# Kernel optimization log

Hardware: AMD Instinct MI355X
Metric: run time of the kernel (lower is better)

The kernel has to match this reference:

```python
import jax, jax.numpy as jnp
import numpy as np

B, S, H = 1, 2048, 2048
NH, NKV, HD = 32, 8, 64
RBS, ICS, RBN = 64, 64, 16          # retrieval_block_size, input_chunk_size, retrieval_block_num
RLEN = RBS * RBN                     # 1024 retrieval tokens
KV = RLEN + S                        # 3072 total kv length
START = RLEN                         # INPUT_START_IDX
SCALE = HD ** -0.5
NEG = -1e9


def _document_ids():
    # mirrors get_document_ids
    ids = np.full(KV, -1, np.int32)
    ids[:START] = np.arange(START) // RBS + 1            # retrieval blocks -> 1..RBN
    chunk = np.arange(S) // ICS
    ids[START:] = np.where(chunk == 0, -1, np.minimum(chunk, RBN))
    return ids


def _block_mask():
    # mirrors causal_retrieval_mask_mod, precomputed dense [S, KV]
    ids = _document_ids()
    qpos = np.arange(S) + START
    kv = np.arange(KV)
    causal = (qpos[:, None] >= kv[None, :]) & (kv[None, :] > START)
    doc = (ids[qpos][:, None] == ids[None, :]) & (kv[None, :] < START)
    return jnp.asarray(causal | doc)


_MASK = _block_mask()


def _rotate_half(x):
    h = x.shape[-1] // 2
    return jnp.concatenate([-x[..., h:], x[..., :h]], axis=-1)


def setup_inputs() -> dict:
    key = jax.random.key(0)
    ks = jax.random.split(key, 6)
    inv_freq = 1.0 / (10000.0 ** (np.arange(0, HD, 2, dtype=np.float32) / HD))
    ang = np.arange(S, dtype=np.float32)[:, None] * inv_freq[None, :]   # [S, HD/2]
    emb = np.concatenate([ang, ang], axis=-1)                            # [S, HD]
    cos = jnp.asarray(np.cos(emb))[None].astype(jnp.float32)            # [1, S, HD]
    sin = jnp.asarray(np.sin(emb))[None].astype(jnp.float32)
    return {
        "hidden_states": jax.random.normal(ks[0], (B, S, H), jnp.float32),
        "cos": cos,
        "sin": sin,
        "retrieval_key": jax.random.normal(ks[1], (B, NKV, RLEN, HD), jnp.float32),
        "retrieval_value": jax.random.normal(ks[2], (B, NKV, RLEN, HD), jnp.float32),
        "Wq": jax.random.normal(ks[3], (H, NH * HD), jnp.float32) * 0.02,
        "Wk": jax.random.normal(ks[4], (H, NKV * HD), jnp.float32) * 0.02,
        "Wv": jax.random.normal(ks[5], (H, NKV * HD), jnp.float32) * 0.02,
        "Wo": jax.random.normal(jax.random.fold_in(key, 7), (NH * HD, H), jnp.float32) * 0.02,
    }


def reference(hidden_states, cos, sin, retrieval_key, retrieval_value, Wq, Wk, Wv, Wo):
    # QKV projections -> [B, nheads, S, HD]
    q = (hidden_states @ Wq).reshape(B, S, NH, HD).transpose(0, 2, 1, 3)
    k = (hidden_states @ Wk).reshape(B, S, NKV, HD).transpose(0, 2, 1, 3)
    v = (hidden_states @ Wv).reshape(B, S, NKV, HD).transpose(0, 2, 1, 3)
    # RoPE (retrieval kv is pre-encoded; rope only on current tokens)
    c, s = cos[:, None, :, :], sin[:, None, :, :]
    q = q * c + _rotate_half(q) * s
    k = k * c + _rotate_half(k) * s
    # prepend retrieval kv
    k = jnp.concatenate([retrieval_key, k], axis=2)    # [B, NKV, KV, HD]
    v = jnp.concatenate([retrieval_value, v], axis=2)
    # GQA: expand kv heads
    g = NH // NKV
    k = jnp.repeat(k, g, axis=1)                        # [B, NH, KV, HD]
    v = jnp.repeat(v, g, axis=1)
    scores = jnp.einsum("bhqd,bhkd->bhqk", q, k) * SCALE
    scores = jnp.where(_MASK[None, None], scores, NEG)
    probs = jax.nn.softmax(scores, axis=-1)
    # fully-masked rows (q_idx 0) -> zero output, matching flex_attention
    row_valid = _MASK.any(axis=-1)[None, None, :, None]
    probs = jnp.where(row_valid, probs, 0.0)
    out = jnp.einsum("bhqk,bhkd->bhqd", probs, v)
    out = out.transpose(0, 2, 1, 3).reshape(B, S, NH * HD)
    return out @ Wo
```

## Files before the change

kernel.cpp:

```cpp
#include <hip/hip_runtime.h>

#define S_LEN 2048
#define H_DIM 2048
#define NH 32
#define NKV 8
#define HD 64
#define RLEN 1024
#define KVTOT 3072
#define SCALE 0.125f
#define QS 0.18033688011112042f
#define FIX8 11.541560327111707f

typedef unsigned short ushort_t;
using short8 = __attribute__((ext_vector_type(8))) short;
using f32x4 = __attribute__((ext_vector_type(4))) float;

__device__ __forceinline__ float b2f(unsigned short u) {
    union { unsigned int i; float f; } v;
    v.i = ((unsigned int)u) << 16;
    return v.f;
}
__device__ __forceinline__ unsigned short f2b(float f) {
    union { float f; unsigned int i; } v;
    v.f = f;
    unsigned int x = v.i;
    return (unsigned short)((x + 0x7fffu + ((x >> 16) & 1u)) >> 16);
}

__device__ __forceinline__ uint4 ld8(const void* A, size_t idx, int F) {
    if (F) {
        const float* p = (const float*)A + idx;
        float4 f0 = ((const float4*)p)[0], f1 = ((const float4*)p)[1];
        ushort_t o[8];
        o[0] = f2b(f0.x); o[1] = f2b(f0.y); o[2] = f2b(f0.z); o[3] = f2b(f0.w);
        o[4] = f2b(f1.x); o[5] = f2b(f1.y); o[6] = f2b(f1.z); o[7] = f2b(f1.w);
        return *(uint4*)o;
    }
    return *(const uint4*)((const ushort_t*)A + idx);
}

__global__ void detect9(const void* p0, const void* p1, const void* p2,
                        const void* p3, const void* p4, const void* p5,
                        const void* p6, const void* p7, const void* p8,
                        int* flags)
{
    __shared__ int bad;
    if (threadIdx.x == 0) bad = 0;
    __syncthreads();
    const void* ps[9] = {p0, p1, p2, p3, p4, p5, p6, p7, p8};
    const unsigned int* w = (const unsigned int*)ps[blockIdx.x];
    int cnt = 0;
    for (int i = threadIdx.x; i < 4096; i += blockDim.x) {
        unsigned int lo = w[i] & 0xFFFFu;
        unsigned int e = (lo >> 7) & 0xFFu;
        if (lo != 0u && (e < 90u || e > 140u)) ++cnt;
    }
    atomicAdd(&bad, cnt);
    __syncthreads();
    if (threadIdx.x == 0) flags[blockIdx.x] = (bad > 16) ? 1 : 0;
}

__global__ __launch_bounds__(256) void cvtW(
    const void* __restrict__ Wq, const void* __restrict__ Wk,
    const void* __restrict__ Wv, const void* __restrict__ Wo,
    ushort_t* __restrict__ WqkvT, ushort_t* __restrict__ WoT,
    const int* __restrict__ flags)
{
    const int z = blockIdx.z;
    if ((z == 1 || z == 2) && blockIdx.x >= 8) return;
    const void* src = (z == 0) ? Wq : (z == 1) ? Wk : (z == 2) ? Wv : Wo;
    const int F = flags[5 + z];
    const int C = (z == 1 || z == 2) ? 512 : 2048;
    ushort_t* dst = (z == 3) ? WoT : WqkvT;
    const int rofs = (z == 1) ? 2048 : (z == 2) ? 2560 : 0;

    __shared__ ushort_t S[64 * 72];
    const int r0 = blockIdx.y * 64, c0 = blockIdx.x * 64;
    const int lr = threadIdx.x >> 2, lc = (threadIdx.x & 3) * 16;
    size_t base = (size_t)(r0 + lr) * C + c0 + lc;
    *(uint4*)&S[lr * 72 + lc] = ld8(src, base, F);
    *(uint4*)&S[lr * 72 + lc + 8] = ld8(src, base + 8, F);
    __syncthreads();
    const int wc = threadIdx.x >> 2, wr = (threadIdx.x & 3) * 16;
    ushort_t o[16];
#pragma unroll
    for (int j = 0; j < 16; ++j) o[j] = S[(wr + j) * 72 + wc];
    ushort_t* q = dst + (size_t)(rofs + c0 + wc) * 2048 + r0 + wr;
    *(uint4*)q = *(const uint4*)o;
    *(uint4*)(q + 8) = *(const uint4*)(o + 8);
}

__global__ __launch_bounds__(256) void gemm_qkv(
    const void* __restrict__ A, const ushort_t* __restrict__ Bt,
    ushort_t* __restrict__ C, int N, int K, const int* __restrict__ aF_)
{
    const int aF = *aF_;
    __shared__ __align__(16) ushort_t As[2][64 * 40];
    __shared__ __align__(16) ushort_t Bs[2][128 * 40];
    const int tid = threadIdx.x;
    const int wave = tid >> 6, lane = tid & 63;
    const int lq = lane & 15, quad = lane >> 4;
    const int m0 = blockIdx.y * 64, n0 = blockIdx.x * 128;
    const int wm = (wave & 1) * 32, wn = (wave >> 1) * 64;
    const int ar = tid >> 2, ak = (tid & 3) * 8;
    const int br = tid >> 1, bk = (tid & 1) * 16;
    const int nk = K >> 5;

    f32x4 acc[2][4];
#pragma unroll
    for (int i = 0; i < 2; ++i)
#pragma unroll
        for (int j = 0; j < 4; ++j) acc[i][j] = (f32x4){0.f, 0.f, 0.f, 0.f};

    const size_t aidx = (size_t)(m0 + ar) * K + ak;
    const ushort_t* bp = Bt + (size_t)(n0 + br) * K + bk;
    {
        uint4 a0 = ld8(A, aidx, aF);
        uint4 b0 = ((const uint4*)bp)[0], b1 = ((const uint4*)bp)[1];
        *(uint4*)&As[0][ar * 40 + ak] = a0;
        *(uint4*)&Bs[0][br * 40 + bk] = b0; *(uint4*)&Bs[0][br * 40 + bk + 8] = b1;
    }

    for (int kt = 0; kt < nk; ++kt) {
        const int cur = kt & 1;
        uint4 na0, nb0, nb1;
        const bool more = (kt + 1 < nk);
        if (more) {
            na0 = ld8(A, aidx + (kt + 1) * 32, aF);
            const ushort_t* bp2 = bp + (kt + 1) * 32;
            nb0 = ((const uint4*)bp2)[0]; nb1 = ((const uint4*)bp2)[1];
        }
        __syncthreads();
        short8 afr[2], bfr[4];
#pragma unroll
        for (int i = 0; i < 2; ++i)
            afr[i] = *(const short8*)&As[cur][(wm + i * 16 + lq) * 40 + quad * 8];
#pragma unroll
        for (int j = 0; j < 4; ++j)
            bfr[j] = *(const short8*)&Bs[cur][(wn + j * 16 + lq) * 40 + quad * 8];
#pragma unroll
        for (int i = 0; i < 2; ++i)
#pragma unroll
            for (int j = 0; j < 4; ++j)
                acc[i][j] = __builtin_amdgcn_mfma_f32_16x16x32_bf16(afr[i], bfr[j], acc[i][j], 0, 0, 0);
        __syncthreads();
        if (more) {
            const int nxt = cur ^ 1;
            *(uint4*)&As[nxt][ar * 40 + ak] = na0;
            *(uint4*)&Bs[nxt][br * 40 + bk] = nb0; *(uint4*)&Bs[nxt][br * 40 + bk + 8] = nb1;
        }
    }

#pragma unroll
    for (int i = 0; i < 2; ++i)
#pragma unroll
        for (int r = 0; r < 4; ++r) {
            ushort_t* cp = C + (size_t)(m0 + wm + i * 16 + quad * 4 + r) * N + n0 + wn + lq;
#pragma unroll
            for (int j = 0; j < 4; ++j) cp[j * 16] = f2b(acc[i][j][r]);
        }
}

__global__ __launch_bounds__(256) void gemm_fin(
    const ushort_t* __restrict__ A, const ushort_t* __restrict__ Bt,
    void* __restrict__ Cv, int N, int K, const int* __restrict__ oF_)
{
    const int oF = *oF_;
    __shared__ __align__(16) ushort_t As[2][64 * 40];
    __shared__ __align__(16) ushort_t Bs[2][128 * 40];
    const int tid = threadIdx.x;
    const int wave = tid >> 6, lane = tid & 63;
    const int lq = lane & 15, quad = lane >> 4;
    const int m0 = blockIdx.y * 64, n0 = blockIdx.x * 128;
    const int wm = (wave & 1) * 32, wn = (wave >> 1) * 64;
    const int ar = tid >> 2, ak = (tid & 3) * 8;
    const int br = tid >> 1, bk = (tid & 1) * 16;
    const int nk = K >> 5;

    f32x4 acc[2][4];
#pragma unroll
    for (int i = 0; i < 2; ++i)
#pragma unroll
        for (int j = 0; j < 4; ++j) acc[i][j] = (f32x4){0.f, 0.f, 0.f, 0.f};

    const ushort_t* ap = A + (size_t)(m0 + ar) * K + ak;
    const ushort_t* bp = Bt + (size_t)(n0 + br) * K + bk;
    {
        uint4 a0 = ((const uint4*)ap)[0];
        uint4 b0 = ((const uint4*)bp)[0], b1 = ((const uint4*)bp)[1];
        *(uint4*)&As[0][ar * 40 + ak] = a0;
        *(uint4*)&Bs[0][br * 40 + bk] = b0; *(uint4*)&Bs[0][br * 40 + bk + 8] = b1;
    }

    for (int kt = 0; kt < nk; ++kt) {
        const int cur = kt & 1;
        uint4 na0, nb0, nb1;
        const bool more = (kt + 1 < nk);
        if (more) {
            na0 = *(const uint4*)(ap + (kt + 1) * 32);
            const ushort_t* bp2 = bp + (kt + 1) * 32;
            nb0 = ((const uint4*)bp2)[0]; nb1 = ((const uint4*)bp2)[1];
        }
        __syncthreads();
        short8 afr[2], bfr[4];
#pragma unroll
        for (int i = 0; i < 2; ++i)
            afr[i] = *(const short8*)&As[cur][(wm + i * 16 + lq) * 40 + quad * 8];
#pragma unroll
        for (int j = 0; j < 4; ++j)
            bfr[j] = *(const short8*)&Bs[cur][(wn + j * 16 + lq) * 40 + quad * 8];
#pragma unroll
        for (int i = 0; i < 2; ++i)
#pragma unroll
            for (int j = 0; j < 4; ++j)
                acc[i][j] = __builtin_amdgcn_mfma_f32_16x16x32_bf16(afr[i], bfr[j], acc[i][j], 0, 0, 0);
        __syncthreads();
        if (more) {
            const int nxt = cur ^ 1;
            *(uint4*)&As[nxt][ar * 40 + ak] = na0;
            *(uint4*)&Bs[nxt][br * 40 + bk] = nb0; *(uint4*)&Bs[nxt][br * 40 + bk + 8] = nb1;
        }
    }

#pragma unroll
    for (int i = 0; i < 2; ++i)
#pragma unroll
        for (int r = 0; r < 4; ++r) {
            size_t off = (size_t)(m0 + wm + i * 16 + quad * 4 + r) * N + n0 + wn + lq;
            if (oF) {
                float* cp = (float*)Cv + off;
#pragma unroll
                for (int j = 0; j < 4; ++j) cp[j * 16] = acc[i][j][r];
            } else {
                ushort_t* cp = (ushort_t*)Cv + off;
#pragma unroll
                for (int j = 0; j < 4; ++j) cp[j * 16] = f2b(acc[i][j][r]);
            }
        }
}

__global__ __launch_bounds__(256) void prepKV(
    const void* __restrict__ rk, const void* __restrict__ rv,
    const ushort_t* __restrict__ qkvp,
    const void* __restrict__ cosv, const void* __restrict__ sinv,
    ushort_t* __restrict__ ktall, ushort_t* __restrict__ vtall,
    const int* __restrict__ flags)
{
    if (blockIdx.z == 0) {
        const int vF = flags[4];
        const int t = blockIdx.x;
        const int kvh = blockIdx.y;
        __shared__ ushort_t S[64 * 72];
        const int lr = threadIdx.x >> 2, lc = (threadIdx.x & 3) * 16;
        if (t < 16) {
            size_t base = ((size_t)kvh * RLEN + t * 64 + lr) * HD + lc;
            *(uint4*)&S[lr * 72 + lc] = ld8(rv, base, vF);
            *(uint4*)&S[lr * 72 + lc + 8] = ld8(rv, base + 8, vF);
        } else {
            const ushort_t* p = qkvp + (size_t)((t - 16) * 64 + lr) * 3072 + 2560 + kvh * HD + lc;
            *(uint4*)&S[lr * 72 + lc] = ((const uint4*)p)[0];
            *(uint4*)&S[lr * 72 + lc + 8] = ((const uint4*)p)[1];
        }
        __syncthreads();
        const int wc = threadIdx.x >> 2, wr = (threadIdx.x & 3) * 16;
        ushort_t o[16];
#pragma unroll
        for (int j = 0; j < 16; ++j) o[j] = S[(wr + j) * 72 + wc];
        const int blk = t * 2 + (wr >> 5);
        ushort_t* q = vtall + (((size_t)(kvh * 96 + blk) * 64 + wc) * 32) + (wr & 31);
        *(uint4*)q = *(const uint4*)o;
        *(uint4*)(q + 8) = *(const uint4*)(o + 8);
    } else {
        const int kF = flags[3], cF = flags[1], sF = flags[2];
        int flat = (blockIdx.y * 48 + blockIdx.x) * 256 + threadIdx.x;
        const int d0 = (flat & 3) * 8;
        const int p = (flat >> 2) % KVTOT;
        const int kvh = (flat >> 2) / KVTOT;
        ushort_t o0[8], o1[8];
        if (p < RLEN) {
            size_t base = ((size_t)kvh * RLEN + p) * HD;
            *(uint4*)o0 = ld8(rk, base + d0, kF);
            *(uint4*)o1 = ld8(rk, base + d0 + 32, kF);
        } else {
            const int si = p - RLEN;
            const ushort_t* s = qkvp + (size_t)si * 3072 + 2048 + kvh * HD;
            uint4 u0 = *(const uint4*)(s + d0);
            uint4 u1 = *(const uint4*)(s + d0 + 32);
            const ushort_t* a16 = (const ushort_t*)&u0;
            const ushort_t* b16 = (const ushort_t*)&u1;
            int ci = si * HD + d0;
            float c0[8], c1[8], s0[8], s1[8];
            if (cF) {
                const float* cp = (const float*)cosv + ci;
#pragma unroll
                for (int j = 0; j < 8; ++j) { c0[j] = cp[j]; c1[j] = cp[j + 32]; }
            } else {
                const ushort_t* cp = (const ushort_t*)cosv + ci;
#pragma unroll
                for (int j = 0; j < 8; ++j) { c0[j] = b2f(cp[j]); c1[j] = b2f(cp[j + 32]); }
            }
            if (sF) {
                const float* sp = (const float*)sinv + ci;
#pragma unroll
                for (int j = 0; j < 8; ++j) { s0[j] = sp[j]; s1[j] = sp[j + 32]; }
            } else {
                const ushort_t* sp = (const ushort_t*)sinv + ci;
#pragma unroll
                for (int j = 0; j < 8; ++j) { s0[j] = b2f(sp[j]); s1[j] = b2f(sp[j + 32]); }
            }
#pragma unroll
            for (int j = 0; j < 8; ++j) {
                float a = b2f(a16[j]), b = b2f(b16[j]);
                o0[j] = f2b(a * c0[j] - b * s0[j]);
                o1[j] = f2b(b * c1[j] + a * s1[j]);
            }
        }
        ushort_t* q = ktall + ((size_t)kvh * KVTOT + p) * HD;
        *(uint4*)(q + d0) = *(const uint4*)o0;
        *(uint4*)(q + d0 + 32) = *(const uint4*)o1;
    }
}

__global__ __launch_bounds__(256) void fattn(
    const ushort_t* __restrict__ qkvp, const ushort_t* __restrict__ ktall,
    const ushort_t* __restrict__ vtall, ushort_t* __restrict__ attno,
    const void* __restrict__ cosv, const void* __restrict__ sinv,
    const int* __restrict__ flags)
{
    const int cF = flags[1], sF = flags[2];
    const int h = blockIdx.x;
    const int qb = 31 - blockIdx.y;
    const int kvh = h >> 2;
    const int tid = threadIdx.x;
    const int wave = tid >> 6;
    const int lane = tid & 63;
    const int lq = lane & 15;
    const int quad = lane >> 4;
    const int rb64 = ((qb < 17 ? qb : 16) - 1) * 64;

    __shared__ __align__(16) ushort_t Ks[128 * 72];
    __shared__ __align__(16) ushort_t Ps[4 * 16 * 136];
    ushort_t* pw = &Ps[wave * 16 * 136];

    short8 qfrag[2];
    {
        const int row_g = qb * 64 + wave * 16 + lq;
        const ushort_t* qrow = qkvp + (size_t)row_g * 3072 + h * HD;
        short8 t0 = *(const short8*)(qrow + quad * 8);
        short8 t1 = *(const short8*)(qrow + 32 + quad * 8);
        const int ci = row_g * HD + quad * 8;
        float c0[8], c1[8], s0[8], s1[8];
        if (cF) {
            const float* cp = (const float*)cosv + ci;
#pragma unroll
            for (int j = 0; j < 8; ++j) { c0[j] = cp[j]; c1[j] = cp[j + 32]; }
        } else {
            const ushort_t* cp = (const ushort_t*)cosv + ci;
#pragma unroll
            for (int j = 0; j < 8; ++j) { c0[j] = b2f(cp[j]); c1[j] = b2f(cp[j + 32]); }
        }
        if (sF) {
            const float* sp = (const float*)sinv + ci;
#pragma unroll
            for (int j = 0; j < 8; ++j) { s0[j] = sp[j]; s1[j] = sp[j + 32]; }
        } else {
            const ushort_t* sp = (const ushort_t*)sinv + ci;
#pragma unroll
            for (int j = 0; j < 8; ++j) { s0[j] = b2f(sp[j]); s1[j] = b2f(sp[j + 32]); }
        }
#pragma unroll
        for (int j = 0; j < 8; ++j) {
            float a = b2f((unsigned short)t0[j]), b = b2f((unsigned short)t1[j]);
            qfrag[0][j] = (short)f2b((a * c0[j] - b * s0[j]) * QS);
            qfrag[1][j] = (short)f2b((b * c1[j] + a * s1[j]) * QS);
        }
    }

    f32x4 oacc[4];
#pragma unroll
    for (int nt = 0; nt < 4; ++nt) oacc[nt] = (f32x4){0.f, 0.f, 0.f, 0.f};
    float lsum[4] = {0.f, 0.f, 0.f, 0.f};

    const int Lq = (qb > 0) ? qb * 64 + 128 : 64;
    const int nch = (Lq + 127) >> 7;
    const ushort_t* kbase = ktall + (size_t)kvh * KVTOT * HD;
    const ushort_t* vbase = vtall + (size_t)kvh * 96 * 2048;

    const int krow = tid >> 1;
    const int kd0 = (tid & 1) * 32;

    uint4 kreg0, kreg1, kreg2, kreg3;
    {
        uint4 z = {0, 0, 0, 0};
        kreg0 = z; kreg1 = z; kreg2 = z; kreg3 = z;
        int p = krow;
        if (p < Lq) {
            int pk = (qb > 0) ? ((p < 64) ? rb64 + p : 960 + p) : RLEN + p;
            const uint4* s = (const uint4*)(kbase + (size_t)pk * HD + kd0);
            kreg0 = s[0]; kreg1 = s[1]; kreg2 = s[2]; kreg3 = s[3];
        }
    }

    for (int c = 0; c < nch; ++c) {
        {
            uint4* dk = (uint4*)&Ks[krow * 72 + kd0];
            dk[0] = kreg0; dk[1] = kreg1; dk[2] = kreg2; dk[3] = kreg3;
        }
        __syncthreads();

        if (c + 1 < nch) {
            uint4 z = {0, 0, 0, 0};
            kreg0 = z; kreg1 = z; kreg2 = z; kreg3 = z;
            int p = (c + 1) * 128 + krow;
            if (p < Lq) {
                int pk = (qb > 0) ? ((p < 64) ? rb64 + p : 960 + p) : RLEN + p;
                const uint4* s = (const uint4*)(kbase + (size_t)pk * HD + kd0);
                kreg0 = s[0]; kreg1 = s[1]; kreg2 = s[2]; kreg3 = s[3];
            }
        }

        int vblk[4];
#pragma unroll
        for (int kc = 0; kc < 4; ++kc) {
            int p = c * 128 + kc * 32;
            int pk = (qb > 0) ? ((p < 64) ? rb64 + p : 960 + p) : RLEN + p;
            if (pk > KVTOT - 1) pk = KVTOT - 1;
            vblk[kc] = pk >> 5;
        }
        short8 vfA[4], vfB[4];
#pragma unroll
        for (int ntd = 0; ntd < 4; ++ntd)
            vfA[ntd] = *(const short8*)(vbase + ((size_t)vblk[0] * 64 + ntd * 16 + lq) * 32 + quad * 8);
#pragma unroll
        for (int ntd = 0; ntd < 4; ++ntd)
            vfB[ntd] = *(const short8*)(vbase + ((size_t)vblk[1] * 64 + ntd * 16 + lq) * 32 + quad * 8);

        const bool lastc = (c == nch - 1) || (qb == 0);
#pragma unroll
        for (int nt = 0; nt < 8; ++nt) {
            f32x4 a = (f32x4){0.f, 0.f, 0.f, 0.f};
            a = __builtin_amdgcn_mfma_f32_16x16x32_bf16(qfrag[0],
                *(const short8*)&Ks[(nt * 16 + lq) * 72 + quad * 8], a, 0, 0, 0);
            a = __builtin_amdgcn_mfma_f32_16x16x32_bf16(qfrag[1],
                *(const short8*)&Ks[(nt * 16 + lq) * 72 + 32 + quad * 8], a, 0, 0, 0);
            const int p = c * 128 + nt * 16 + lq;
#pragma unroll
            for (int r = 0; r < 4; ++r) {
                float pexp = exp2f(a[r] - FIX8);
                if (lastc) {
                    const int qg = qb * 64 + wave * 16 + quad * 4 + r;
                    bool valid;
                    if (qb > 0) valid = (p < 64) || ((p - 64) >= 1 && (p - 64) <= qg);
                    else        valid = (p >= 1 && p <= qg);
                    if (!valid) pexp = 0.f;
                } else if (c == 0) {
                    if (p == 64) pexp = 0.f;
                }
                lsum[r] += pexp;
                pw[(quad * 4 + r) * 136 + nt * 16 + lq] = f2b(pexp);
            }
        }

#pragma unroll
        for (int kc = 0; kc < 4; ++kc) {
            short8 pa = *(const short8*)&pw[lq * 136 + kc * 32 + quad * 8];
            short8 vf0, vf1, vf2, vf3;
            if (kc == 0)      { vf0 = vfA[0]; vf1 = vfA[1]; vf2 = vfA[2]; vf3 = vfA[3]; }
            else if (kc == 1) { vf0 = vfB[0]; vf1 = vfB[1]; vf2 = vfB[2]; vf3 = vfB[3]; }
            else {
                const int b = vblk[kc];
                vf0 = *(const short8*)(vbase + ((size_t)b * 64 + 0 * 16 + lq) * 32 + quad * 8);
                vf1 = *(const short8*)(vbase + ((size_t)b * 64 + 1 * 16 + lq) * 32 + quad * 8);
                vf2 = *(const short8*)(vbase + ((size_t)b * 64 + 2 * 16 + lq) * 32 + quad * 8);
                vf3 = *(const short8*)(vbase + ((size_t)b * 64 + 3 * 16 + lq) * 32 + quad * 8);
            }
            oacc[0] = __builtin_amdgcn_mfma_f32_16x16x32_bf16(pa, vf0, oacc[0], 0, 0, 0);
            oacc[1] = __builtin_amdgcn_mfma_f32_16x16x32_bf16(pa, vf1, oacc[1], 0, 0, 0);
            oacc[2] = __builtin_amdgcn_mfma_f32_16x16x32_bf16(pa, vf2, oacc[2], 0, 0, 0);
            oacc[3] = __builtin_amdgcn_mfma_f32_16x16x32_bf16(pa, vf3, oacc[3], 0, 0, 0);
        }
        __syncthreads();
    }

#pragma unroll
    for (int r = 0; r < 4; ++r) {
        float v = lsum[r];
        v += __shfl_xor(v, 1, 64); v += __shfl_xor(v, 2, 64);
        v += __shfl_xor(v, 4, 64); v += __shfl_xor(v, 8, 64);
        lsum[r] = v;
    }
#pragma unroll
    for (int r = 0; r < 4; ++r) {
        const int qg = qb * 64 + wave * 16 + quad * 4 + r;
        const float inv = (qg == 0) ? 0.f : 1.f / lsum[r];
        ushort_t* orow = attno + (size_t)qg * 2048 + h * HD;
#pragma unroll
        for (int nt = 0; nt < 4; ++nt)
            orow[nt * 16 + lq] = f2b(oacc[nt][r] * inv);
    }
}

extern "C" void kernel_launch(void* const* d_in, const int* in_sizes, int n_in,
                              void* d_out, int out_size, void* d_ws, size_t ws_size,
                              hipStream_t stream) {
    const void* hs   = d_in[0];
    const void* cosv = d_in[1];
    const void* sinv = d_in[2];
    const void* rk   = d_in[3];
    const void* rv   = d_in[4];
    const void* Wq   = d_in[5];
    const void* Wk   = d_in[6];
    const void* Wv   = d_in[7];
    const void* Wo   = d_in[8];

    char* ws = (char*)d_ws;
    int*      flags  = (int*)ws;
    ushort_t* ktall  = (ushort_t*)(ws + (1u  << 20));
    ushort_t* vtall  = (ushort_t*)(ws + (1u << 20) + (13u << 18));
    ushort_t* WqkvT  = (ushort_t*)(ws + (9u  << 20));
    ushort_t* attno  = WqkvT;
    ushort_t* WoT    = (ushort_t*)(ws + (21u << 20));
    ushort_t* qkvp   = (ushort_t*)(ws + (29u << 20));

    detect9<<<9, 256, 0, stream>>>(hs, cosv, sinv, rk, rv, Wq, Wk, Wv, Wo, flags);

    cvtW<<<dim3(32, 32, 4), 256, 0, stream>>>(Wq, Wk, Wv, Wo, WqkvT, WoT, flags);

    gemm_qkv<<<dim3(3072 / 128, 2048 / 64), 256, 0, stream>>>(hs, WqkvT, qkvp, 3072, 2048, flags + 0);

    prepKV<<<dim3(48, 8, 2), 256, 0, stream>>>(rk, rv, qkvp, cosv, sinv, ktall, vtall, flags);

    fattn<<<dim3(NH, 32), 256, 0, stream>>>(qkvp, ktall, vtall, attno, cosv, sinv, flags);

    gemm_fin<<<dim3(2048 / 128, 2048 / 64), 256, 0, stream>>>(attno, WoT, d_out, 2048, 2048, flags + 0);
}
```

Before: 288.6 us.

## Split long query blocks' KV range across two workgroups with a reduce kernel

Query blocks 16..31, which have the longest KV ranges, are each split into two workgroups that process halves of the KV chunks. One half writes unnormalized partial outputs into attno and the other into a scratch buffer, and both write their row sums to Lbuf. A new freduce kernel then adds the partials and normalizes them. This balances per-workgroup work and raises the workgroup count, at the cost of an extra launch, partial outputs rounded to bf16, and the loss of the register prefetch of the next K chunk, which is now loaded synchronously each iteration. The fixed exponent offset in place of a running max makes combining the partials by simple addition valid.

```diff
diff --git a/kernel.cpp b/kernel.cpp
--- a/kernel.cpp
+++ b/kernel.cpp
@@ -324,12 +324,31 @@
 __global__ __launch_bounds__(256) void fattn(
     const ushort_t* __restrict__ qkvp, const ushort_t* __restrict__ ktall,
     const ushort_t* __restrict__ vtall, ushort_t* __restrict__ attno,
+    ushort_t* __restrict__ part, float* __restrict__ Lbuf,
     const void* __restrict__ cosv, const void* __restrict__ sinv,
     const int* __restrict__ flags)
 {
     const int cF = flags[1], sF = flags[2];
     const int h = blockIdx.x;
-    const int qb = 31 - blockIdx.y;
+    const int y = blockIdx.y;
+    int qb, cBeg, cEnd, split, slice;
+    {
+        if (y < 32) {
+            qb = 31 - (y >> 1);
+            slice = y & 1;
+            split = 1;
+            const int nch = ((qb * 64 + 128) + 127) >> 7;
+            const int half = nch >> 1;
+            cBeg = slice ? half : 0;
+            cEnd = slice ? nch : half;
+        } else {
+            qb = 47 - y;
+            slice = 0; split = 0;
+            cBeg = 0;
+            cEnd = (qb > 0) ? (((qb * 64 + 128) + 127) >> 7) : 1;
+        }
+    }
+    const int nchTot = (qb > 0) ? (((qb * 64 + 128) + 127) >> 7) : 1;
     const int kvh = h >> 2;
     const int tid = threadIdx.x;
     const int wave = tid >> 6;
@@ -382,43 +401,23 @@
     float lsum[4] = {0.f, 0.f, 0.f, 0.f};
 
     const int Lq = (qb > 0) ? qb * 64 + 128 : 64;
-    const int nch = (Lq + 127) >> 7;
     const ushort_t* kbase = ktall + (size_t)kvh * KVTOT * HD;
     const ushort_t* vbase = vtall + (size_t)kvh * 96 * 2048;
 
-    const int krow = tid >> 1;
-    const int kd0 = (tid & 1) * 32;
-
-    uint4 kreg0, kreg1, kreg2, kreg3;
-    {
-        uint4 z = {0, 0, 0, 0};
-        kreg0 = z; kreg1 = z; kreg2 = z; kreg3 = z;
-        int p = krow;
-        if (p < Lq) {
-            int pk = (qb > 0) ? ((p < 64) ? rb64 + p : 960 + p) : RLEN + p;
-            const uint4* s = (const uint4*)(kbase + (size_t)pk * HD + kd0);
-            kreg0 = s[0]; kreg1 = s[1]; kreg2 = s[2]; kreg3 = s[3];
-        }
-    }
-
-    for (int c = 0; c < nch; ++c) {
+    for (int c = cBeg; c < cEnd; ++c) {
+        uint4 kreg0, kreg1, kreg2, kreg3;
+        const int krow = tid >> 1;
+        const int kd0 = (tid & 1) * 32;
         {
-            uint4* dk = (uint4*)&Ks[krow * 72 + kd0];
-            dk[0] = kreg0; dk[1] = kreg1; dk[2] = kreg2; dk[3] = kreg3;
-        }
-        __syncthreads();
-
-        if (c + 1 < nch) {
+            int p = c * 128 + krow;
             uint4 z = {0, 0, 0, 0};
             kreg0 = z; kreg1 = z; kreg2 = z; kreg3 = z;
-            int p = (c + 1) * 128 + krow;
             if (p < Lq) {
                 int pk = (qb > 0) ? ((p < 64) ? rb64 + p : 960 + p) : RLEN + p;
                 const uint4* s = (const uint4*)(kbase + (size_t)pk * HD + kd0);
                 kreg0 = s[0]; kreg1 = s[1]; kreg2 = s[2]; kreg3 = s[3];
             }
         }
-
         int vblk[4];
 #pragma unroll
         for (int kc = 0; kc < 4; ++kc) {
@@ -435,7 +434,13 @@
         for (int ntd = 0; ntd < 4; ++ntd)
             vfB[ntd] = *(const short8*)(vbase + ((size_t)vblk[1] * 64 + ntd * 16 + lq) * 32 + quad * 8);
 
-        const bool lastc = (c == nch - 1) || (qb == 0);
+        {
+            uint4* dk = (uint4*)&Ks[krow * 72 + kd0];
+            dk[0] = kreg0; dk[1] = kreg1; dk[2] = kreg2; dk[3] = kreg3;
+        }
+        __syncthreads();
+
+        const bool lastc = (c == nchTot - 1) || (qb == 0);
 #pragma unroll
         for (int nt = 0; nt < 8; ++nt) {
             f32x4 a = (f32x4){0.f, 0.f, 0.f, 0.f};
@@ -489,15 +494,58 @@
         v += __shfl_xor(v, 4, 64); v += __shfl_xor(v, 8, 64);
         lsum[r] = v;
     }
-#pragma unroll
-    for (int r = 0; r < 4; ++r) {
-        const int qg = qb * 64 + wave * 16 + quad * 4 + r;
-        const float inv = (qg == 0) ? 0.f : 1.f / lsum[r];
-        ushort_t* orow = attno + (size_t)qg * 2048 + h * HD;
-#pragma unroll
-        for (int nt = 0; nt < 4; ++nt)
-            orow[nt * 16 + lq] = f2b(oacc[nt][r] * inv);
-    }
+    if (!split) {
+#pragma unroll
+        for (int r = 0; r < 4; ++r) {
+            const int qg = qb * 64 + wave * 16 + quad * 4 + r;
+            const float inv = (qg == 0) ? 0.f : 1.f / lsum[r];
+            ushort_t* orow = attno + (size_t)qg * 2048 + h * HD;
+#pragma unroll
+            for (int nt = 0; nt < 4; ++nt)
+                orow[nt * 16 + lq] = f2b(oacc[nt][r] * inv);
+        }
+    } else {
+        const int pidx = h * 16 + (qb - 16);
+#pragma unroll
+        for (int r = 0; r < 4; ++r) {
+            const int row = wave * 16 + quad * 4 + r;
+            ushort_t* orow = slice ? (part + (size_t)pidx * 4096 + row * 64)
+                                   : (attno + (size_t)(qb * 64 + row) * 2048 + h * HD);
+#pragma unroll
+            for (int nt = 0; nt < 4; ++nt)
+                orow[nt * 16 + lq] = f2b(oacc[nt][r]);
+            if (lq == 0)
+                Lbuf[(pidx * 2 + slice) * 64 + row] = lsum[r];
+        }
+    }
+}
+
+__global__ __launch_bounds__(256) void freduce(
+    ushort_t* __restrict__ attno, const ushort_t* __restrict__ part,
+    const float* __restrict__ Lbuf)
+{
+    const int idx = blockIdx.x;
+    const int h = idx >> 4;
+    const int qb = 16 + (idx & 15);
+    const int row = threadIdx.x >> 2, d0 = (threadIdx.x & 3) * 16;
+    const float l = Lbuf[idx * 128 + row] + Lbuf[idx * 128 + 64 + row];
+    const float inv = 1.f / l;
+    ushort_t* ap = attno + (size_t)(qb * 64 + row) * 2048 + h * HD + d0;
+    const ushort_t* pp = part + (size_t)idx * 4096 + row * 64 + d0;
+    uint4 a0 = ((const uint4*)ap)[0], a1 = ((const uint4*)ap)[1];
+    uint4 b0 = ((const uint4*)pp)[0], b1 = ((const uint4*)pp)[1];
+    const ushort_t* a16 = (const ushort_t*)&a0;
+    const ushort_t* a16b = (const ushort_t*)&a1;
+    const ushort_t* p16 = (const ushort_t*)&b0;
+    const ushort_t* p16b = (const ushort_t*)&b1;
+    ushort_t o[16];
+#pragma unroll
+    for (int j = 0; j < 8; ++j) {
+        o[j] = f2b((b2f(a16[j]) + b2f(p16[j])) * inv);
+        o[j + 8] = f2b((b2f(a16b[j]) + b2f(p16b[j])) * inv);
+    }
+    *(uint4*)ap = *(const uint4*)o;
+    *(uint4*)(ap + 8) = *(const uint4*)(o + 8);
 }
 
 extern "C" void kernel_launch(void* const* d_in, const int* in_sizes, int n_in,
@@ -515,10 +563,12 @@
 
     char* ws = (char*)d_ws;
     int*      flags  = (int*)ws;
+    float*    Lbuf   = (float*)(ws + (16u << 10));
     ushort_t* ktall  = (ushort_t*)(ws + (1u  << 20));
     ushort_t* vtall  = (ushort_t*)(ws + (1u << 20) + (13u << 18));
     ushort_t* WqkvT  = (ushort_t*)(ws + (9u  << 20));
     ushort_t* attno  = WqkvT;
+    ushort_t* part   = (ushort_t*)(ws + (17u << 20));
     ushort_t* WoT    = (ushort_t*)(ws + (21u << 20));
     ushort_t* qkvp   = (ushort_t*)(ws + (29u << 20));
 
@@ -530,7 +580,9 @@
 
     prepKV<<<dim3(48, 8, 2), 256, 0, stream>>>(rk, rv, qkvp, cosv, sinv, ktall, vtall, flags);
 
-    fattn<<<dim3(NH, 32), 256, 0, stream>>>(qkvp, ktall, vtall, attno, cosv, sinv, flags);
+    fattn<<<dim3(NH, 48), 256, 0, stream>>>(qkvp, ktall, vtall, attno, part, Lbuf, cosv, sinv, flags);
+
+    freduce<<<512, 256, 0, stream>>>(attno, part, Lbuf);
 
     gemm_fin<<<dim3(2048 / 128, 2048 / 64), 256, 0, stream>>>(attno, WoT, d_out, 2048, 2048, flags + 0);
 }
```

After: 294.9 us. 2.2% more time.

## Triple-buffer GEMM shared tiles and drop K register prefetch in attention

Applied to the files above, without the earlier changes.

Both GEMM kernels move from a two-buffer LDS pipeline with two barriers per k-step to a three-buffer ring that needs one barrier per step. Global loads for step k+2 are issued after the barrier so they overlap the MFMA work on the current tile. In the attention kernel, the cross-chunk register prefetch of K is removed. Each chunk now loads K, issues the V fragment loads, then stores K to LDS and syncs, which lowers register pressure but gives up overlap of the K load with the previous chunk's compute.

```diff
diff --git a/kernel.cpp b/kernel.cpp
--- a/kernel.cpp
+++ b/kernel.cpp
@@ -95,8 +95,8 @@
     ushort_t* __restrict__ C, int N, int K, const int* __restrict__ aF_)
 {
     const int aF = *aF_;
-    __shared__ __align__(16) ushort_t As[2][64 * 40];
-    __shared__ __align__(16) ushort_t Bs[2][128 * 40];
+    __shared__ __align__(16) ushort_t As[3][64 * 40];
+    __shared__ __align__(16) ushort_t Bs[3][128 * 40];
     const int tid = threadIdx.x;
     const int wave = tid >> 6, lane = tid & 63;
     const int lq = lane & 15, quad = lane >> 4;
@@ -114,23 +114,32 @@
 
     const size_t aidx = (size_t)(m0 + ar) * K + ak;
     const ushort_t* bp = Bt + (size_t)(n0 + br) * K + bk;
+
     {
         uint4 a0 = ld8(A, aidx, aF);
         uint4 b0 = ((const uint4*)bp)[0], b1 = ((const uint4*)bp)[1];
         *(uint4*)&As[0][ar * 40 + ak] = a0;
         *(uint4*)&Bs[0][br * 40 + bk] = b0; *(uint4*)&Bs[0][br * 40 + bk + 8] = b1;
     }
-
+    uint4 ra, rb0, rb1;
+    {
+        ra = ld8(A, aidx + 32, aF);
+        const ushort_t* bp2 = bp + 32;
+        rb0 = ((const uint4*)bp2)[0]; rb1 = ((const uint4*)bp2)[1];
+    }
+
+    int cur = 0, nxt = 1;
     for (int kt = 0; kt < nk; ++kt) {
-        const int cur = kt & 1;
-        uint4 na0, nb0, nb1;
-        const bool more = (kt + 1 < nk);
-        if (more) {
-            na0 = ld8(A, aidx + (kt + 1) * 32, aF);
-            const ushort_t* bp2 = bp + (kt + 1) * 32;
-            nb0 = ((const uint4*)bp2)[0]; nb1 = ((const uint4*)bp2)[1];
+        if (kt + 1 < nk) {
+            *(uint4*)&As[nxt][ar * 40 + ak] = ra;
+            *(uint4*)&Bs[nxt][br * 40 + bk] = rb0; *(uint4*)&Bs[nxt][br * 40 + bk + 8] = rb1;
         }
         __syncthreads();
+        if (kt + 2 < nk) {
+            ra = ld8(A, aidx + (size_t)(kt + 2) * 32, aF);
+            const ushort_t* bp2 = bp + (kt + 2) * 32;
+            rb0 = ((const uint4*)bp2)[0]; rb1 = ((const uint4*)bp2)[1];
+        }
         short8 afr[2], bfr[4];
 #pragma unroll
         for (int i = 0; i < 2; ++i)
@@ -143,12 +152,8 @@
 #pragma unroll
             for (int j = 0; j < 4; ++j)
                 acc[i][j] = __builtin_amdgcn_mfma_f32_16x16x32_bf16(afr[i], bfr[j], acc[i][j], 0, 0, 0);
-        __syncthreads();
-        if (more) {
-            const int nxt = cur ^ 1;
-            *(uint4*)&As[nxt][ar * 40 + ak] = na0;
-            *(uint4*)&Bs[nxt][br * 40 + bk] = nb0; *(uint4*)&Bs[nxt][br * 40 + bk + 8] = nb1;
-        }
+        cur = nxt;
+        nxt = (nxt == 2) ? 0 : nxt + 1;
     }
 
 #pragma unroll
@@ -166,8 +171,8 @@
     void* __restrict__ Cv, int N, int K, const int* __restrict__ oF_)
 {
     const int oF = *oF_;
-    __shared__ __align__(16) ushort_t As[2][64 * 40];
-    __shared__ __align__(16) ushort_t Bs[2][128 * 40];
+    __shared__ __align__(16) ushort_t As[3][64 * 40];
+    __shared__ __align__(16) ushort_t Bs[3][128 * 40];
     const int tid = threadIdx.x;
     const int wave = tid >> 6, lane = tid & 63;
     const int lq = lane & 15, quad = lane >> 4;
@@ -185,23 +190,32 @@
 
     const ushort_t* ap = A + (size_t)(m0 + ar) * K + ak;
     const ushort_t* bp = Bt + (size_t)(n0 + br) * K + bk;
+
     {
-        uint4 a0 = ((const uint4*)ap)[0];
+        uint4 a0 = *(const uint4*)ap;
         uint4 b0 = ((const uint4*)bp)[0], b1 = ((const uint4*)bp)[1];
         *(uint4*)&As[0][ar * 40 + ak] = a0;
         *(uint4*)&Bs[0][br * 40 + bk] = b0; *(uint4*)&Bs[0][br * 40 + bk + 8] = b1;
     }
-
+    uint4 ra, rb0, rb1;
+    {
+        ra = *(const uint4*)(ap + 32);
+        const ushort_t* bp2 = bp + 32;
+        rb0 = ((const uint4*)bp2)[0]; rb1 = ((const uint4*)bp2)[1];
+    }
+
+    int cur = 0, nxt = 1;
     for (int kt = 0; kt < nk; ++kt) {
-        const int cur = kt & 1;
-        uint4 na0, nb0, nb1;
-        const bool more = (kt + 1 < nk);
-        if (more) {
-            na0 = *(const uint4*)(ap + (kt + 1) * 32);
-            const ushort_t* bp2 = bp + (kt + 1) * 32;
-            nb0 = ((const uint4*)bp2)[0]; nb1 = ((const uint4*)bp2)[1];
+        if (kt + 1 < nk) {
+            *(uint4*)&As[nxt][ar * 40 + ak] = ra;
+            *(uint4*)&Bs[nxt][br * 40 + bk] = rb0; *(uint4*)&Bs[nxt][br * 40 + bk + 8] = rb1;
         }
         __syncthreads();
+        if (kt + 2 < nk) {
+            ra = *(const uint4*)(ap + (size_t)(kt + 2) * 32);
+            const ushort_t* bp2 = bp + (kt + 2) * 32;
+            rb0 = ((const uint4*)bp2)[0]; rb1 = ((const uint4*)bp2)[1];
+        }
         short8 afr[2], bfr[4];
 #pragma unroll
         for (int i = 0; i < 2; ++i)
@@ -214,12 +228,8 @@
 #pragma unroll
             for (int j = 0; j < 4; ++j)
                 acc[i][j] = __builtin_amdgcn_mfma_f32_16x16x32_bf16(afr[i], bfr[j], acc[i][j], 0, 0, 0);
-        __syncthreads();
-        if (more) {
-            const int nxt = cur ^ 1;
-            *(uint4*)&As[nxt][ar * 40 + ak] = na0;
-            *(uint4*)&Bs[nxt][br * 40 + bk] = nb0; *(uint4*)&Bs[nxt][br * 40 + bk + 8] = nb1;
-        }
+        cur = nxt;
+        nxt = (nxt == 2) ? 0 : nxt + 1;
     }
 
 #pragma unroll
@@ -386,39 +396,20 @@
     const ushort_t* kbase = ktall + (size_t)kvh * KVTOT * HD;
     const ushort_t* vbase = vtall + (size_t)kvh * 96 * 2048;
 
-    const int krow = tid >> 1;
-    const int kd0 = (tid & 1) * 32;
-
-    uint4 kreg0, kreg1, kreg2, kreg3;
-    {
-        uint4 z = {0, 0, 0, 0};
-        kreg0 = z; kreg1 = z; kreg2 = z; kreg3 = z;
-        int p = krow;
-        if (p < Lq) {
-            int pk = (qb > 0) ? ((p < 64) ? rb64 + p : 960 + p) : RLEN + p;
-            const uint4* s = (const uint4*)(kbase + (size_t)pk * HD + kd0);
-            kreg0 = s[0]; kreg1 = s[1]; kreg2 = s[2]; kreg3 = s[3];
-        }
-    }
-
     for (int c = 0; c < nch; ++c) {
+        uint4 kreg0, kreg1, kreg2, kreg3;
+        const int krow = tid >> 1;
+        const int kd0 = (tid & 1) * 32;
         {
-            uint4* dk = (uint4*)&Ks[krow * 72 + kd0];
-            dk[0] = kreg0; dk[1] = kreg1; dk[2] = kreg2; dk[3] = kreg3;
-        }
-        __syncthreads();
-
-        if (c + 1 < nch) {
+            int p = c * 128 + krow;
             uint4 z = {0, 0, 0, 0};
             kreg0 = z; kreg1 = z; kreg2 = z; kreg3 = z;
-            int p = (c + 1) * 128 + krow;
             if (p < Lq) {
                 int pk = (qb > 0) ? ((p < 64) ? rb64 + p : 960 + p) : RLEN + p;
                 const uint4* s = (const uint4*)(kbase + (size_t)pk * HD + kd0);
                 kreg0 = s[0]; kreg1 = s[1]; kreg2 = s[2]; kreg3 = s[3];
             }
         }
-
         int vblk[4];
 #pragma unroll
         for (int kc = 0; kc < 4; ++kc) {
@@ -434,6 +425,12 @@
 #pragma unroll
         for (int ntd = 0; ntd < 4; ++ntd)
             vfB[ntd] = *(const short8*)(vbase + ((size_t)vblk[1] * 64 + ntd * 16 + lq) * 32 + quad * 8);
+
+        {
+            uint4* dk = (uint4*)&Ks[krow * 72 + kd0];
+            dk[0] = kreg0; dk[1] = kreg1; dk[2] = kreg2; dk[3] = kreg3;
+        }
+        __syncthreads();
 
         const bool lastc = (c == nch - 1) || (qb == 0);
 #pragma unroll
```

Result: slower. 295.9 us (+2.5%).
